# Performance work log

Measured on AMD Instinct MI355X. Metric: run time of the kernel, lower is better.

## Reference

```python
import jax, jax.numpy as jnp
import numpy as np
import math

N, E, R = 50000, 800000, 32
DIN = 128
H, D = 8, 16          # num_heads, head_dim; H*D == out_ent_feats == 128
HOP = 5
ALPHA = 0.1
EPS = 1e-5


def layer_norm(x, g, b):
    m = jnp.mean(x, axis=-1, keepdims=True)
    v = jnp.mean((x - m) ** 2, axis=-1, keepdims=True)
    return (x - m) * jax.lax.rsqrt(v + EPS) * g + b


def segment_softmax(e, dst, num_nodes):
    # e: [E, H] scores, softmax over incoming edges of each dst node
    m = jax.ops.segment_max(e, dst, num_segments=num_nodes)      # [N, H]
    ex = jnp.exp(e - m[dst])
    s = jax.ops.segment_sum(ex, dst, num_segments=num_nodes)     # [N, H]
    return ex / s[dst]


def setup_inputs() -> dict:
    key = jax.random.key(0)
    ks = jax.random.split(key, 12)
    gain = 0.02  # small init scale (small_init_gain-style)
    ent_feat = jax.random.normal(ks[0], (N, DIN), dtype=jnp.float32)
    rel_feat = jax.random.normal(ks[1], (R, DIN), dtype=jnp.float32)
    src = jax.random.randint(ks[2], (E,), 0, N, dtype=jnp.int32)
    # guarantee every node has in-degree >= 1 (DGL raises otherwise)
    dst_rand = jax.random.randint(ks[3], (E - N,), 0, N, dtype=jnp.int32)
    dst = jnp.concatenate([jnp.arange(N, dtype=jnp.int32), dst_rand])
    rid = jax.random.randint(ks[4], (E,), 0, R, dtype=jnp.int32)
    W_head = jax.random.normal(ks[5], (DIN, H * D), dtype=jnp.float32) * gain
    W_tail = jax.random.normal(ks[6], (DIN, H * D), dtype=jnp.float32) * gain
    W_ent = jax.random.normal(ks[7], (DIN, H * D), dtype=jnp.float32) * gain
    W_rel = jax.random.normal(ks[8], (DIN, H * D), dtype=jnp.float32) * gain
    attn_r = jax.random.normal(ks[9], (1, H, D), dtype=jnp.float32) * gain
    W1 = jax.random.normal(ks[10], (H * D, 4 * H * D), dtype=jnp.float32) * gain
    W2 = jax.random.normal(ks[11], (4 * H * D, H * D), dtype=jnp.float32) * gain
    return dict(
        ent_feat=ent_feat, rel_feat=rel_feat, src=src, dst=dst, rid=rid,
        W_head=W_head, W_tail=W_tail, W_ent=W_ent, W_rel=W_rel, attn_r=attn_r,
        ln_ent_g=jnp.ones((DIN,), jnp.float32), ln_ent_b=jnp.zeros((DIN,), jnp.float32),
        ln_rel_g=jnp.ones((DIN,), jnp.float32), ln_rel_b=jnp.zeros((DIN,), jnp.float32),
        ff_ln_g=jnp.ones((H * D,), jnp.float32), ff_ln_b=jnp.zeros((H * D,), jnp.float32),
        W1=W1, b1=jnp.zeros((4 * H * D,), jnp.float32),
        W2=W2, b2=jnp.zeros((H * D,), jnp.float32),
    )


def _forward(ent_feat, rel_feat, src, dst, rid,
             W_head, W_tail, W_ent, W_rel, attn_r,
             ln_ent_g, ln_ent_b, ln_rel_g, ln_rel_b, ff_ln_g, ff_ln_b,
             W1, b1, W2, b2):
    n = ent_feat.shape[0]
    x = layer_norm(ent_feat, ln_ent_g, ln_ent_b)
    feat_head = (x @ W_head).reshape(n, H, D)
    feat_tail = (x @ W_tail).reshape(n, H, D)
    feat_ent = (x @ W_ent).reshape(n, H, D)

    # per-edge dot-product attention score: u_dot_v('eh','et')
    e = jnp.sum(feat_head[src] * feat_tail[dst], axis=-1)          # [E, H]

    r = layer_norm(rel_feat, ln_rel_g, ln_rel_b)
    feat_rel = (r @ W_rel).reshape(R, H, D)
    er = jnp.sum(feat_rel * attn_r, axis=-1)                       # [R, H]
    e = e * er[rid]                                                # [E, H]

    # e_mul_v with log_in = log(in_degree) of dst node
    deg = jax.ops.segment_sum(jnp.ones((e.shape[0],), e.dtype), dst, num_segments=n)
    log_in = jnp.log(jnp.maximum(deg, 1.0))                        # [N]
    e = e * log_in[dst][:, None] / math.sqrt(D)

    a = segment_softmax(e, dst, n)                                 # [E, H]

    # PPR diffusion: feat <- (1-alpha) * A^T feat + alpha * feat_0
    feat = feat_ent
    for _ in range(HOP):
        msg = feat[src] * a[:, :, None]                            # [E, H, D]
        agg = jax.ops.segment_sum(msg, dst, num_segments=n)        # [N, H, D]
        feat = (1.0 - ALPHA) * agg + ALPHA * feat_ent

    # residual (Identity: in_ent_feats == out_ent_feats)
    rst = feat + ent_feat.reshape(n, H, D)
    rst = rst.reshape(n, H * D)

    h = layer_norm(rst, ff_ln_g, ff_ln_b)
    ff = jax.nn.relu(h @ W1 + b1) @ W2 + b2
    return ff + rst


def reference(ent_feat, rel_feat, src, dst, rid,
              W_head, W_tail, W_ent, W_rel, attn_r,
              ln_ent_g, ln_ent_b, ln_rel_g, ln_rel_b, ff_ln_g, ff_ln_b,
              W1, b1, W2, b2):
    return _forward(ent_feat, rel_feat, src, dst, rid,
                    W_head, W_tail, W_ent, W_rel, attn_r,
                    ln_ent_g, ln_ent_b, ln_rel_g, ln_rel_b, ff_ln_g, ff_ln_b,
                    W1, b1, W2, b2)
```

## Files before the change

### kernel.cpp

```cpp
#include <hip/hip_runtime.h>
#include <hip/hip_bf16.h>

#define N_NODES 50000
#define N_EDGES 800000
#define N_REL 32
#define DIN 128
#define NH 8
#define HD 16
#define FF_HID 512
#define EPS_LN 1e-5f
#define NBUCK 8
#define BDIV 6250
#define BCAP 114688

typedef __attribute__((ext_vector_type(8))) short bf16x8;
typedef __attribute__((ext_vector_type(4))) float f32x4;
typedef __attribute__((ext_vector_type(2))) float f32x2;
typedef unsigned short ushort_t;
typedef unsigned int uint_t;

static __device__ __forceinline__ unsigned short f2bf(float f) {
    union { float f; unsigned u; } v; v.f = f;
    unsigned r = (v.u + 0x7fffu + ((v.u >> 16) & 1u)) >> 16;
    return (unsigned short)r;
}
static __device__ __forceinline__ float bf2f(unsigned u16) {
    union { unsigned u; float f; } v; v.u = u16 << 16; return v.f;
}
static __device__ __forceinline__ unsigned char f2fp8(float f) {
    return (unsigned char)(__builtin_amdgcn_cvt_pk_fp8_f32(f, f, 0, false) & 0xff);
}
static __device__ __forceinline__ uint_t f2fp8x2(float x0, float x1) {
    return (__builtin_amdgcn_cvt_pk_fp8_f32(x0, x1, 0, false) & 0xffffu);
}

static __device__ __forceinline__ void pack_dev(const float* __restrict__ W,
                                                short* __restrict__ out, int K, int Ncols,
                                                int idx) {
    int KT = K >> 5;
    int l = idx & 63;
    int tile = idx >> 6;
    int kt = tile & (KT - 1);
    int ct = tile / KT;
    int c = ct * 16 + (l & 15);
    int k0 = kt * 32 + ((l >> 4) * 8);
    bf16x8 v;
#pragma unroll
    for (int j = 0; j < 8; j++) v[j] = (short)f2bf(W[(size_t)(k0 + j) * Ncols + c]);
    *(bf16x8*)(out + (size_t)idx * 8) = v;
}

#define C0_BIN 512
__global__ __launch_bounds__(256) void combo0_kernel(
    const int* __restrict__ src, const int* __restrict__ dst, const int* __restrict__ rid,
    int* __restrict__ deg, int* __restrict__ gcnt, int2* __restrict__ buck,
    const float* __restrict__ W1, short* __restrict__ W1p, const float* __restrict__ W2,
    short* __restrict__ W2p, const float* __restrict__ Wh, short* __restrict__ Whp,
    const float* __restrict__ Wt, short* __restrict__ Wtp, const float* __restrict__ We,
    short* __restrict__ Wep, const float* __restrict__ rel_feat,
    const float* __restrict__ gr, const float* __restrict__ br,
    const float* __restrict__ W_rel, const float* __restrict__ attn_r,
    float* __restrict__ er) {
    __shared__ float red[128];
    __shared__ float xsr[128];
    __shared__ float prod[128];
    __shared__ int cnt[NBUCK];
    __shared__ int sbase[NBUCK];
    int b = blockIdx.x, tid = threadIdx.x;
    if (b < C0_BIN) {
        const int chunk = (N_EDGES + C0_BIN - 1) / C0_BIN;
        int i0 = b * chunk;
        int i1 = min(i0 + chunk, N_EDGES);
        int rounds = (i1 - i0 + 255) >> 8;
        for (int r = 0; r < rounds; r++) {
            int i = i0 + (r << 8) + tid;
            if (tid < NBUCK) cnt[tid] = 0;
            __syncthreads();
            int d = 0, b8 = 0, rank = 0, py = 0;
            bool v = i < i1;
            if (v) {
                d = dst[i];
                b8 = d / BDIV;
                py = src[i] | (rid[i] << 16);
                rank = atomicAdd(&cnt[b8], 1);
                atomicAdd(&deg[d], 1);
            }
            __syncthreads();
            if (tid < NBUCK) sbase[tid] = atomicAdd(&gcnt[tid], cnt[tid]);
            __syncthreads();
            if (v) buck[(size_t)b8 * BCAP + sbase[b8] + rank] = make_int2(d, py);
            __syncthreads();
        }
    } else if (b < C0_BIN + 32) {
        pack_dev(W1, W1p, DIN, FF_HID, (b - C0_BIN) * 256 + tid);
    } else if (b < C0_BIN + 64) {
        pack_dev(W2, W2p, FF_HID, DIN, (b - C0_BIN - 32) * 256 + tid);
    } else if (b < C0_BIN + 72) {
        pack_dev(Wh, Whp, DIN, DIN, (b - C0_BIN - 64) * 256 + tid);
    } else if (b < C0_BIN + 80) {
        pack_dev(Wt, Wtp, DIN, DIN, (b - C0_BIN - 72) * 256 + tid);
    } else if (b < C0_BIN + 88) {
        pack_dev(We, Wep, DIN, DIN, (b - C0_BIN - 80) * 256 + tid);
    } else {
        int r = b - (C0_BIN + 88);
        float x = 0.f;
        if (tid < 128) {
            x = rel_feat[r * DIN + tid];
            red[tid] = x;
        }
        __syncthreads();
        for (int off = 64; off > 0; off >>= 1) {
            if (tid < off) red[tid] += red[tid + off];
            __syncthreads();
        }
        float mean = red[0] * (1.f / DIN);
        __syncthreads();
        if (tid < 128) red[tid] = x * x;
        __syncthreads();
        for (int off = 64; off > 0; off >>= 1) {
            if (tid < off) red[tid] += red[tid + off];
            __syncthreads();
        }
        float var = red[0] * (1.f / DIN) - mean * mean;
        float rs = rsqrtf(var + EPS_LN);
        if (tid < 128) xsr[tid] = (x - mean) * rs * gr[tid] + br[tid];
        __syncthreads();
        if (tid < 128) {
            float acc = 0.f;
            for (int k = 0; k < DIN; k++) acc += xsr[k] * W_rel[k * DIN + tid];
            prod[tid] = acc * attn_r[tid];
        }
        __syncthreads();
        if (tid < NH) {
            float s = 0.f;
            for (int d = 0; d < HD; d++) s += prod[tid * HD + d];
            er[r * NH + tid] = s;
        }
    }
}

__global__ __launch_bounds__(1024) void scan2_kernel(const int* __restrict__ deg,
                                                     int* __restrict__ row_off, int n) {
    __shared__ int lds[1024];
    __shared__ int wsum[16];
    __shared__ int s_base;
    int b = blockIdx.x, tid = threadIdx.x;
    int start = b * 1024;
    int partial = 0;
    for (int i = tid; i < start; i += 1024) partial += deg[i];
    for (int m = 32; m > 0; m >>= 1) partial += __shfl_down(partial, m);
    int wid = tid >> 6, lane = tid & 63;
    if (lane == 0) wsum[wid] = partial;
    __syncthreads();
    if (tid == 0) {
        int s = 0;
#pragma unroll
        for (int w = 0; w < 16; w++) s += wsum[w];
        s_base = s;
    }
    int i = start + tid;
    int v = (i < n) ? deg[i] : 0;
    lds[tid] = v;
    __syncthreads();
    for (int off = 1; off < 1024; off <<= 1) {
        int t = (tid >= off) ? lds[tid - off] : 0;
        __syncthreads();
        lds[tid] += t;
        __syncthreads();
    }
    int base = s_base;
    if (i < n) row_off[i] = base + lds[tid] - v;
    if (i == n - 1) row_off[n] = base + lds[tid];
}

#define C1_SCAT 1024
__global__ __launch_bounds__(256) void combo1_kernel(
    const int2* __restrict__ buck, const int* __restrict__ gcnt,
    const int* __restrict__ row_off, int* __restrict__ cursor, int* __restrict__ sr_perm,
    const float* __restrict__ ent, const float* __restrict__ g, const float* __restrict__ b,
    const short* __restrict__ Whp, const short* __restrict__ Wtp,
    const short* __restrict__ Wep, unsigned char* __restrict__ head_fp8,
    ushort_t* __restrict__ tail_bf, ushort_t* __restrict__ entp_bf,
    unsigned char* __restrict__ entp_fp8) {
    __shared__ float xs[32][128];
    __shared__ short hsb[32][136];
    int blk = blockIdx.x, tid = threadIdx.x;
    if (blk < C1_SCAT) {
        int b8 = blk & 7, sub = blk >> 3;
        int cnt = gcnt[b8];
        int chunk = (cnt + 127) >> 7;
        int i0 = sub * chunk;
        int i1 = min(i0 + chunk, cnt);
        const int2* bp = buck + (size_t)b8 * BCAP;
        for (int i = i0 + tid; i < i1; i += 256) {
            int2 e = bp[i];
            int p = row_off[e.x] + atomicAdd(&cursor[e.x], 1);
            sr_perm[p] = e.y;
        }
        return;
    }
    int base = (blk - C1_SCAT) * 32;
    {
        int c = tid & 127, rb = tid >> 7;
#pragma unroll
        for (int j = 0; j < 16; j++) {
            int r = j * 2 + rb;
            int row = base + r;
            xs[r][c] = (row < N_NODES) ? ent[(size_t)row * DIN + c] : 0.f;
        }
    }
    __syncthreads();
    int wave = tid >> 6, lane = tid & 63;
    {
        float g0 = g[lane], g1 = g[lane + 64], bb0 = b[lane], bb1 = b[lane + 64];
        for (int r = wave * 8; r < wave * 8 + 8; r++) {
            float x0 = xs[r][lane], x1 = xs[r][lane + 64];
            float s1 = x0 + x1, s2 = x0 * x0 + x1 * x1;
            for (int m = 1; m < 64; m <<= 1) {
                s1 += __shfl_xor(s1, m);
                s2 += __shfl_xor(s2, m);
            }
            float mean = s1 * (1.f / DIN);
            float var = s2 * (1.f / DIN) - mean * mean;
            float rs = rsqrtf(var + EPS_LN);
            hsb[r][lane] = (short)f2bf((x0 - mean) * rs * g0 + bb0);
            hsb[r][lane + 64] = (short)f2bf((x1 - mean) * rs * g1 + bb1);
        }
    }
    __syncthreads();
    bf16x8 a[2][4];
#pragma unroll
    for (int rt = 0; rt < 2; rt++)
#pragma unroll
        for (int kt = 0; kt < 4; kt++)
            a[rt][kt] = *(const bf16x8*)&hsb[rt * 16 + (lane & 15)][kt * 32 + (lane >> 4) * 8];
#pragma unroll
    for (int m = 0; m < 3; m++) {
        const bf16x8* bp = (m == 0)   ? (const bf16x8*)Whp
                           : (m == 1) ? (const bf16x8*)Wtp
                                      : (const bf16x8*)Wep;
#pragma unroll
        for (int c2 = 0; c2 < 2; c2++) {
            int ct = wave * 2 + c2;
            f32x4 acc0 = {0.f, 0.f, 0.f, 0.f}, acc1 = {0.f, 0.f, 0.f, 0.f};
#pragma unroll
            for (int kt = 0; kt < 4; kt++) {
                bf16x8 bf = bp[(ct * 4 + kt) * 64 + lane];
                acc0 = __builtin_amdgcn_mfma_f32_16x16x32_bf16(a[0][kt], bf, acc0, 0, 0, 0);
                acc1 = __builtin_amdgcn_mfma_f32_16x16x32_bf16(a[1][kt], bf, acc1, 0, 0, 0);
            }
            int col = ct * 16 + (lane & 15);
            int r0 = (lane >> 4) * 4;
#pragma unroll
            for (int j = 0; j < 4; j++) {
                int row0 = base + r0 + j, row1 = base + 16 + r0 + j;
                if (m == 0) {
                    if (row0 < N_NODES) head_fp8[(size_t)row0 * DIN + col] = f2fp8(acc0[j]);
                    if (row1 < N_NODES) head_fp8[(size_t)row1 * DIN + col] = f2fp8(acc1[j]);
                } else if (m == 1) {
                    if (row0 < N_NODES) tail_bf[(size_t)row0 * DIN + col] = f2bf(acc0[j]);
                    if (row1 < N_NODES) tail_bf[(size_t)row1 * DIN + col] = f2bf(acc1[j]);
                } else {
                    if (row0 < N_NODES) {
                        entp_bf[(size_t)row0 * DIN + col] = f2bf(acc0[j]);
                        entp_fp8[(size_t)row0 * DIN + col] = f2fp8(acc0[j]);
                    }
                    if (row1 < N_NODES) {
                        entp_bf[(size_t)row1 * DIN + col] = f2bf(acc1[j]);
                        entp_fp8[(size_t)row1 * DIN + col] = f2fp8(acc1[j]);
                    }
                }
            }
        }
    }
}

__global__ __launch_bounds__(256) void scores_kernel(
    const unsigned char* __restrict__ head_fp8, const ushort_t* __restrict__ tail_bf,
    const float* __restrict__ er, const int* __restrict__ row_off,
    const int* __restrict__ sr_perm, ushort_t* __restrict__ a_bf,
    float* __restrict__ inv9) {
    int wid = threadIdx.x >> 6;
    int u = blockIdx.x * 4 + wid;
    int lane = threadIdx.x & 63;
    int h = lane & 7, esub = lane >> 3;
    int p0 = row_off[u], p1 = row_off[u + 1];
    int deg = p1 - p0;
    float scale = logf((float)(deg > 0 ? deg : 1)) * 0.25f;
    float t[16];
    {
        const uint_t* tp = (const uint_t*)(tail_bf + (size_t)u * DIN + h * HD);
#pragma unroll
        for (int i = 0; i < 8; i++) {
            uint_t w = tp[i];
            t[2 * i] = bf2f(w & 0xffffu);
            t[2 * i + 1] = bf2f(w >> 16);
        }
    }
    float ssum = 0.f;
    for (int p = p0 + esub; p < p1; p += 8) {
        int v = sr_perm[p];
        int s = v & 0xffff;
        int rr = v >> 16;
        const uint_t* hp = (const uint_t*)(head_fp8 + (size_t)s * DIN + h * HD);
        float dot = 0.f;
#pragma unroll
        for (int i = 0; i < 4; i++) {
            uint_t w = hp[i];
            f32x2 lo = __builtin_amdgcn_cvt_pk_f32_fp8(w, false);
            f32x2 hi = __builtin_amdgcn_cvt_pk_f32_fp8(w, true);
            dot += lo.x * t[4 * i] + lo.y * t[4 * i + 1] + hi.x * t[4 * i + 2] +
                   hi.y * t[4 * i + 3];
        }
        float e = dot * er[rr * NH + h] * scale;
        float sx = expf(e);
        a_bf[(size_t)p * NH + h] = f2bf(sx);
        ssum += sx;
    }
    ssum += __shfl_xor(ssum, 8);
    ssum += __shfl_xor(ssum, 16);
    ssum += __shfl_xor(ssum, 32);
    if (lane < 8) inv9[(size_t)u * NH + lane] = 0.9f / ssum;
}

template <bool OUT_BF>
__global__ __launch_bounds__(256) void diffuse4_kernel(
    const unsigned char* __restrict__ fin8, const ushort_t* __restrict__ entp_bf,
    const ushort_t* __restrict__ a_bf, const int* __restrict__ sr_perm,
    const int* __restrict__ row_off, const float* __restrict__ inv9,
    void* __restrict__ fout) {
    int wid = threadIdx.x >> 6;
    int u = blockIdx.x * 4 + wid;
    int lane = threadIdx.x & 63;
    int c = lane & 15;
    int g = lane >> 4;
    int hh = c >> 1;
    int p0 = row_off[u], p1 = row_off[u + 1];
    float acc[8];
#pragma unroll
    for (int j = 0; j < 8; j++) acc[j] = 0.f;
    for (int p = p0; p < p1; p += 4) {
        int pe = p + g;
        bool valid = pe < p1;
        int pc = valid ? pe : (p1 - 1);
        int s = sr_perm[pc] & 0xffff;
        float a = valid ? bf2f(a_bf[(size_t)pc * NH + hh]) : 0.f;
        uint2 w = *(const uint2*)(fin8 + (size_t)s * DIN + 8 * c);
        f32x2 l0 = __builtin_amdgcn_cvt_pk_f32_fp8(w.x, false);
        f32x2 h0 = __builtin_amdgcn_cvt_pk_f32_fp8(w.x, true);
        f32x2 l1 = __builtin_amdgcn_cvt_pk_f32_fp8(w.y, false);
        f32x2 h1 = __builtin_amdgcn_cvt_pk_f32_fp8(w.y, true);
        acc[0] += a * l0.x; acc[1] += a * l0.y; acc[2] += a * h0.x; acc[3] += a * h0.y;
        acc[4] += a * l1.x; acc[5] += a * l1.y; acc[6] += a * h1.x; acc[7] += a * h1.y;
    }
#pragma unroll
    for (int j = 0; j < 8; j++) {
        acc[j] += __shfl_xor(acc[j], 16);
        acc[j] += __shfl_xor(acc[j], 32);
    }
    if (g == 0) {
        float iv = inv9[(size_t)u * NH + hh];
        size_t o = (size_t)u * DIN + 8 * c;
        uint4 e4 = *(const uint4*)(entp_bf + o);
        float x0 = iv * acc[0] + 0.1f * bf2f(e4.x & 0xffffu);
        float x1 = iv * acc[1] + 0.1f * bf2f(e4.x >> 16);
        float x2 = iv * acc[2] + 0.1f * bf2f(e4.y & 0xffffu);
        float x3 = iv * acc[3] + 0.1f * bf2f(e4.y >> 16);
        float x4 = iv * acc[4] + 0.1f * bf2f(e4.z & 0xffffu);
        float x5 = iv * acc[5] + 0.1f * bf2f(e4.z >> 16);
        float x6 = iv * acc[6] + 0.1f * bf2f(e4.w & 0xffffu);
        float x7 = iv * acc[7] + 0.1f * bf2f(e4.w >> 16);
        if (OUT_BF) {
            uint4 ov;
            ov.x = (uint_t)f2bf(x0) | ((uint_t)f2bf(x1) << 16);
            ov.y = (uint_t)f2bf(x2) | ((uint_t)f2bf(x3) << 16);
            ov.z = (uint_t)f2bf(x4) | ((uint_t)f2bf(x5) << 16);
            ov.w = (uint_t)f2bf(x6) | ((uint_t)f2bf(x7) << 16);
            *(uint4*)((ushort_t*)fout + o) = ov;
        } else {
            uint2 ov;
            ov.x = f2fp8x2(x0, x1) | (f2fp8x2(x2, x3) << 16);
            ov.y = f2fp8x2(x4, x5) | (f2fp8x2(x6, x7) << 16);
            *(uint2*)((unsigned char*)fout + o) = ov;
        }
    }
}

static __device__ __forceinline__ int hid_idx(int row, int col) {
    return row * 512 + ((((col >> 3) & 63) ^ (row & 7)) << 3) + (col & 7);
}
__global__ __launch_bounds__(256) void ffn_mfma_kernel(
    const ushort_t* __restrict__ feat, const float* __restrict__ ent0,
    const float* __restrict__ g, const float* __restrict__ b,
    const short* __restrict__ W1p, const float* __restrict__ b1,
    const short* __restrict__ W2p, const float* __restrict__ b2,
    float* __restrict__ out) {
    __shared__ ushort_t rst_bf[16][136];
    __shared__ short hs[16][136];
    __shared__ short hid[16 * 512];
    int tid = threadIdx.x;
    int base = blockIdx.x * 16;
    int wave = tid >> 6, lane = tid & 63;
    {
        int c = tid & 127, rb = tid >> 7;
#pragma unroll
        for (int j = 0; j < 8; j++) {
            int r = j * 2 + rb;
            int row = base + r;
            float v = 0.f;
            if (row < N_NODES) {
                size_t idx = (size_t)row * DIN + c;
                v = bf2f(feat[idx]) + ent0[idx];
            }
            rst_bf[r][c] = f2bf(v);
        }
    }
    __syncthreads();
    {
        float g0 = g[lane], g1 = g[lane + 64], bb0 = b[lane], bb1 = b[lane + 64];
        for (int r = wave * 4; r < wave * 4 + 4; r++) {
            float x0 = bf2f(rst_bf[r][lane]), x1 = bf2f(rst_bf[r][lane + 64]);
            float s1 = x0 + x1, s2 = x0 * x0 + x1 * x1;
            for (int m = 1; m < 64; m <<= 1) {
                s1 += __shfl_xor(s1, m);
                s2 += __shfl_xor(s2, m);
            }
            float mean = s1 * (1.f / DIN);
            float var = s2 * (1.f / DIN) - mean * mean;
            float rs = rsqrtf(var + EPS_LN);
            hs[r][lane] = (short)f2bf((x0 - mean) * rs * g0 + bb0);
            hs[r][lane + 64] = (short)f2bf((x1 - mean) * rs * g1 + bb1);
        }
    }
    __syncthreads();
    {
        bf16x8 a[4];
#pragma unroll
        for (int kt = 0; kt < 4; kt++)
            a[kt] = *(const bf16x8*)&hs[lane & 15][kt * 32 + (lane >> 4) * 8];
        const bf16x8* bp = (const bf16x8*)W1p;
        for (int cti = 0; cti < 8; cti++) {
            int ct = wave * 8 + cti;
            f32x4 acc0 = {0.f, 0.f, 0.f, 0.f};
#pragma unroll
            for (int kt = 0; kt < 4; kt++) {
                bf16x8 bf = bp[(ct * 4 + kt) * 64 + lane];
                acc0 = __builtin_amdgcn_mfma_f32_16x16x32_bf16(a[kt], bf, acc0, 0, 0, 0);
            }
            int col = ct * 16 + (lane & 15);
            float bv = b1[col];
            int r0 = (lane >> 4) * 4;
#pragma unroll
            for (int j = 0; j < 4; j++)
                hid[hid_idx(r0 + j, col)] = (short)f2bf(fmaxf(acc0[j] + bv, 0.f));
        }
    }
    __syncthreads();
    {
        f32x4 acc[2] = {{0.f, 0.f, 0.f, 0.f}, {0.f, 0.f, 0.f, 0.f}};
        const bf16x8* bp2 = (const bf16x8*)W2p;
        for (int kt = 0; kt < 16; kt++) {
            int col8 = kt * 32 + (lane >> 4) * 8;
            bf16x8 a0 = *(const bf16x8*)&hid[hid_idx(lane & 15, col8)];
#pragma unroll
            for (int c2 = 0; c2 < 2; c2++) {
                int ct = wave * 2 + c2;
                bf16x8 bf = bp2[(ct * 16 + kt) * 64 + lane];
                acc[c2] = __builtin_amdgcn_mfma_f32_16x16x32_bf16(a0, bf, acc[c2], 0, 0, 0);
            }
        }
#pragma unroll
        for (int c2 = 0; c2 < 2; c2++) {
            int col = (wave * 2 + c2) * 16 + (lane & 15);
            float bv = b2[col];
            int r0 = (lane >> 4) * 4;
#pragma unroll
            for (int j = 0; j < 4; j++) {
                int row = base + r0 + j;
                if (row < N_NODES)
                    out[(size_t)row * DIN + col] = acc[c2][j] + bv + bf2f(rst_bf[r0 + j][col]);
            }
        }
    }
}

extern "C" void kernel_launch(void* const* d_in, const int* in_sizes, int n_in,
                              void* d_out, int out_size, void* d_ws, size_t ws_size,
                              hipStream_t stream) {
    const float* ent_feat = (const float*)d_in[0];
    const float* rel_feat = (const float*)d_in[1];
    const int* src = (const int*)d_in[2];
    const int* dst = (const int*)d_in[3];
    const int* rid = (const int*)d_in[4];
    const float* W_head = (const float*)d_in[5];
    const float* W_tail = (const float*)d_in[6];
    const float* W_ent = (const float*)d_in[7];
    const float* W_rel = (const float*)d_in[8];
    const float* attn_r = (const float*)d_in[9];
    const float* ln_ent_g = (const float*)d_in[10];
    const float* ln_ent_b = (const float*)d_in[11];
    const float* ln_rel_g = (const float*)d_in[12];
    const float* ln_rel_b = (const float*)d_in[13];
    const float* ff_ln_g = (const float*)d_in[14];
    const float* ff_ln_b = (const float*)d_in[15];
    const float* W1 = (const float*)d_in[16];
    const float* b1 = (const float*)d_in[17];
    const float* W2 = (const float*)d_in[18];
    const float* b2 = (const float*)d_in[19];
    float* out = (float*)d_out;

    const int N = N_NODES, E = N_EDGES;

    char* cur = (char*)d_ws;
    auto alloc = [&](size_t bytes, size_t align) -> void* {
        uintptr_t p = (uintptr_t)cur;
        p = (p + align - 1) & ~(uintptr_t)(align - 1);
        cur = (char*)(p + bytes);
        return (void*)p;
    };
    ushort_t* tail_bf = (ushort_t*)alloc((size_t)N * DIN * 2, 16);
    ushort_t* entp_bf = (ushort_t*)alloc((size_t)N * DIN * 2, 16);
    unsigned char* entp_fp8 = (unsigned char*)alloc((size_t)N * DIN, 16);
    unsigned char* f8A = (unsigned char*)alloc((size_t)N * DIN, 16);
    unsigned char* f8B = (unsigned char*)alloc((size_t)N * DIN, 16);
    unsigned char* head_fp8 = (unsigned char*)alloc((size_t)N * DIN, 16);
    int2* buck = (int2*)alloc((size_t)NBUCK * BCAP * 8, 16);
    int* sr_perm = (int*)alloc((size_t)E * 4, 16);
    int* row_off = (int*)alloc((size_t)(N + 1) * 4, 16);
    int* deg = (int*)alloc(((size_t)2 * N + NBUCK) * 4, 16);
    int* cursor = deg + N;
    int* gcnt = deg + 2 * N;
    float* er = (float*)alloc((size_t)N_REL * NH * 4, 16);
    float* inv9 = (float*)alloc((size_t)N * NH * 4, 16);
    short* W1p = (short*)alloc((size_t)DIN * FF_HID * 2, 16);
    short* W2p = (short*)alloc((size_t)FF_HID * DIN * 2, 16);
    short* Whp = (short*)alloc((size_t)DIN * DIN * 2, 16);
    short* Wtp = (short*)alloc((size_t)DIN * DIN * 2, 16);
    short* Wep = (short*)alloc((size_t)DIN * DIN * 2, 16);
    ushort_t* a_fit = (ushort_t*)alloc((size_t)E * NH * 2, 16);
    ushort_t* a_bf = ((size_t)(cur - (char*)d_ws) <= ws_size) ? a_fit : (ushort_t*)d_out;

    hipMemsetAsync(deg, 0, sizeof(int) * ((size_t)2 * N + NBUCK), stream);
    combo0_kernel<<<632, 256, 0, stream>>>(src, dst, rid, deg, gcnt, buck, W1, W1p, W2,
                                           W2p, W_head, Whp, W_tail, Wtp, W_ent, Wep,
                                           rel_feat, ln_rel_g, ln_rel_b, W_rel, attn_r,
                                           er);
    scan2_kernel<<<(N + 1023) / 1024, 1024, 0, stream>>>(deg, row_off, N);
    int nblk32 = (N + 31) / 32;
    combo1_kernel<<<C1_SCAT + nblk32, 256, 0, stream>>>(
        buck, gcnt, row_off, cursor, sr_perm, ent_feat, ln_ent_g, ln_ent_b, Whp, Wtp,
        Wep, head_fp8, tail_bf, entp_bf, entp_fp8);
    scores_kernel<<<N / 4, 256, 0, stream>>>(head_fp8, tail_bf, er, row_off, sr_perm,
                                             a_bf, inv9);
    diffuse4_kernel<false><<<N / 4, 256, 0, stream>>>(entp_fp8, entp_bf, a_bf, sr_perm,
                                                      row_off, inv9, f8A);
    diffuse4_kernel<false><<<N / 4, 256, 0, stream>>>(f8A, entp_bf, a_bf, sr_perm,
                                                      row_off, inv9, f8B);
    diffuse4_kernel<false><<<N / 4, 256, 0, stream>>>(f8B, entp_bf, a_bf, sr_perm,
                                                      row_off, inv9, f8A);
    diffuse4_kernel<false><<<N / 4, 256, 0, stream>>>(f8A, entp_bf, a_bf, sr_perm,
                                                      row_off, inv9, f8B);
    diffuse4_kernel<true><<<N / 4, 256, 0, stream>>>(f8B, entp_bf, a_bf, sr_perm,
                                                     row_off, inv9, tail_bf);
    int nblk16 = (N + 15) / 16;
    ffn_mfma_kernel<<<nblk16, 256, 0, stream>>>(tail_bf, ent_feat, ff_ln_g, ff_ln_b, W1p,
                                                b1, W2p, b2, out);
}
```

Baseline: 369.2 us.

## Fuse first diffusion hop into score kernel and interleave head/ent fp8 layout

```diff
diff --git a/kernel.cpp b/kernel.cpp
--- a/kernel.cpp
+++ b/kernel.cpp
@@ -32,6 +32,11 @@
 }
 static __device__ __forceinline__ uint_t f2fp8x2(float x0, float x1) {
     return (__builtin_amdgcn_cvt_pk_fp8_f32(x0, x1, 0, false) & 0xffffu);
+}
+static __device__ __forceinline__ void fp8x4_to_f32(uint_t w, float* o) {
+    f32x2 lo = __builtin_amdgcn_cvt_pk_f32_fp8(w, false);
+    f32x2 hi = __builtin_amdgcn_cvt_pk_f32_fp8(w, true);
+    o[0] = lo.x; o[1] = lo.y; o[2] = hi.x; o[3] = hi.y;
 }
 
 static __device__ __forceinline__ void pack_dev(const float* __restrict__ W,
@@ -139,67 +144,43 @@
     }
 }
 
-__global__ __launch_bounds__(1024) void scan2_kernel(const int* __restrict__ deg,
-                                                     int* __restrict__ row_off, int n) {
-    __shared__ int lds[1024];
-    __shared__ int wsum[16];
-    __shared__ int s_base;
-    int b = blockIdx.x, tid = threadIdx.x;
-    int start = b * 1024;
-    int partial = 0;
-    for (int i = tid; i < start; i += 1024) partial += deg[i];
-    for (int m = 32; m > 0; m >>= 1) partial += __shfl_down(partial, m);
-    int wid = tid >> 6, lane = tid & 63;
-    if (lane == 0) wsum[wid] = partial;
-    __syncthreads();
-    if (tid == 0) {
-        int s = 0;
-#pragma unroll
-        for (int w = 0; w < 16; w++) s += wsum[w];
-        s_base = s;
-    }
-    int i = start + tid;
-    int v = (i < n) ? deg[i] : 0;
-    lds[tid] = v;
-    __syncthreads();
-    for (int off = 1; off < 1024; off <<= 1) {
-        int t = (tid >= off) ? lds[tid - off] : 0;
-        __syncthreads();
-        lds[tid] += t;
-        __syncthreads();
-    }
-    int base = s_base;
-    if (i < n) row_off[i] = base + lds[tid] - v;
-    if (i == n - 1) row_off[n] = base + lds[tid];
-}
-
-#define C1_SCAT 1024
-__global__ __launch_bounds__(256) void combo1_kernel(
-    const int2* __restrict__ buck, const int* __restrict__ gcnt,
-    const int* __restrict__ row_off, int* __restrict__ cursor, int* __restrict__ sr_perm,
+#define NS_SCAN 196
+__global__ __launch_bounds__(256) void combo_mid_kernel(
+    const int* __restrict__ deg, int* __restrict__ row_off,
     const float* __restrict__ ent, const float* __restrict__ g, const float* __restrict__ b,
     const short* __restrict__ Whp, const short* __restrict__ Wtp,
-    const short* __restrict__ Wep, unsigned char* __restrict__ head_fp8,
-    ushort_t* __restrict__ tail_bf, ushort_t* __restrict__ entp_bf,
-    unsigned char* __restrict__ entp_fp8) {
+    const short* __restrict__ Wep, unsigned char* __restrict__ hent,
+    ushort_t* __restrict__ tail_bf) {
     __shared__ float xs[32][128];
     __shared__ short hsb[32][136];
     int blk = blockIdx.x, tid = threadIdx.x;
-    if (blk < C1_SCAT) {
-        int b8 = blk & 7, sub = blk >> 3;
-        int cnt = gcnt[b8];
-        int chunk = (cnt + 127) >> 7;
-        int i0 = sub * chunk;
-        int i1 = min(i0 + chunk, cnt);
-        const int2* bp = buck + (size_t)b8 * BCAP;
-        for (int i = i0 + tid; i < i1; i += 256) {
-            int2 e = bp[i];
-            int p = row_off[e.x] + atomicAdd(&cursor[e.x], 1);
-            sr_perm[p] = e.y;
-        }
+    if (blk < NS_SCAN) {
+        __shared__ int lscan[256];
+        __shared__ int ws4[4];
+        int n = N_NODES;
+        int start = blk * 256;
+        int partial = 0;
+        for (int i = tid; i < start; i += 256) partial += deg[i];
+        for (int m = 32; m > 0; m >>= 1) partial += __shfl_down(partial, m);
+        int wid = tid >> 6, lane = tid & 63;
+        if (lane == 0) ws4[wid] = partial;
+        __syncthreads();
+        int sbase = ws4[0] + ws4[1] + ws4[2] + ws4[3];
+        int i = start + tid;
+        int v = (i < n) ? deg[i] : 0;
+        lscan[tid] = v;
+        __syncthreads();
+        for (int off = 1; off < 256; off <<= 1) {
+            int t = (tid >= off) ? lscan[tid - off] : 0;
+            __syncthreads();
+            lscan[tid] += t;
+            __syncthreads();
+        }
+        if (i < n) row_off[i] = sbase + lscan[tid] - v;
+        if (i == n - 1) row_off[n] = sbase + lscan[tid];
         return;
     }
-    int base = (blk - C1_SCAT) * 32;
+    int base = (blk - NS_SCAN) * 32;
     {
         int c = tid & 127, rb = tid >> 7;
 #pragma unroll
@@ -250,36 +231,50 @@
                 acc1 = __builtin_amdgcn_mfma_f32_16x16x32_bf16(a[1][kt], bf, acc1, 0, 0, 0);
             }
             int col = ct * 16 + (lane & 15);
+            int h = col >> 4, k = col & 15;
             int r0 = (lane >> 4) * 4;
 #pragma unroll
             for (int j = 0; j < 4; j++) {
                 int row0 = base + r0 + j, row1 = base + 16 + r0 + j;
                 if (m == 0) {
-                    if (row0 < N_NODES) head_fp8[(size_t)row0 * DIN + col] = f2fp8(acc0[j]);
-                    if (row1 < N_NODES) head_fp8[(size_t)row1 * DIN + col] = f2fp8(acc1[j]);
+                    if (row0 < N_NODES) hent[(size_t)row0 * 256 + h * 32 + k] = f2fp8(acc0[j]);
+                    if (row1 < N_NODES) hent[(size_t)row1 * 256 + h * 32 + k] = f2fp8(acc1[j]);
                 } else if (m == 1) {
                     if (row0 < N_NODES) tail_bf[(size_t)row0 * DIN + col] = f2bf(acc0[j]);
                     if (row1 < N_NODES) tail_bf[(size_t)row1 * DIN + col] = f2bf(acc1[j]);
                 } else {
-                    if (row0 < N_NODES) {
-                        entp_bf[(size_t)row0 * DIN + col] = f2bf(acc0[j]);
-                        entp_fp8[(size_t)row0 * DIN + col] = f2fp8(acc0[j]);
-                    }
-                    if (row1 < N_NODES) {
-                        entp_bf[(size_t)row1 * DIN + col] = f2bf(acc1[j]);
-                        entp_fp8[(size_t)row1 * DIN + col] = f2fp8(acc1[j]);
-                    }
+                    if (row0 < N_NODES)
+                        hent[(size_t)row0 * 256 + h * 32 + 16 + k] = f2fp8(acc0[j]);
+                    if (row1 < N_NODES)
+                        hent[(size_t)row1 * 256 + h * 32 + 16 + k] = f2fp8(acc1[j]);
                 }
             }
         }
     }
 }
 
-__global__ __launch_bounds__(256) void scores_kernel(
-    const unsigned char* __restrict__ head_fp8, const ushort_t* __restrict__ tail_bf,
+__global__ __launch_bounds__(256) void scatter_kernel(
+    const int2* __restrict__ buck, const int* __restrict__ gcnt,
+    const int* __restrict__ row_off, int* __restrict__ cursor, int* __restrict__ sr_perm) {
+    int blk = blockIdx.x, tid = threadIdx.x;
+    int b8 = blk & 7, sub = blk >> 3;
+    int cnt = gcnt[b8];
+    int chunk = (cnt + 127) >> 7;
+    int i0 = sub * chunk;
+    int i1 = min(i0 + chunk, cnt);
+    const int2* bp = buck + (size_t)b8 * BCAP;
+    for (int i = i0 + tid; i < i1; i += 256) {
+        int2 e = bp[i];
+        int p = row_off[e.x] + atomicAdd(&cursor[e.x], 1);
+        sr_perm[p] = e.y;
+    }
+}
+
+__global__ __launch_bounds__(256) void score_hop_kernel(
+    const unsigned char* __restrict__ hent, const ushort_t* __restrict__ tail_bf,
     const float* __restrict__ er, const int* __restrict__ row_off,
     const int* __restrict__ sr_perm, ushort_t* __restrict__ a_bf,
-    float* __restrict__ inv9) {
+    float* __restrict__ inv9, unsigned char* __restrict__ fout) {
     int wid = threadIdx.x >> 6;
     int u = blockIdx.x * 4 + wid;
     int lane = threadIdx.x & 63;
@@ -298,34 +293,62 @@
         }
     }
     float ssum = 0.f;
+    float acc[16];
+#pragma unroll
+    for (int k = 0; k < 16; k++) acc[k] = 0.f;
     for (int p = p0 + esub; p < p1; p += 8) {
         int v = sr_perm[p];
         int s = v & 0xffff;
         int rr = v >> 16;
-        const uint_t* hp = (const uint_t*)(head_fp8 + (size_t)s * DIN + h * HD);
+        const uint4* hp = (const uint4*)(hent + (size_t)s * 256 + h * 32);
+        uint4 hw = hp[0];
+        uint4 ew = hp[1];
+        float hv[16], ev[16];
+        fp8x4_to_f32(hw.x, hv + 0); fp8x4_to_f32(hw.y, hv + 4);
+        fp8x4_to_f32(hw.z, hv + 8); fp8x4_to_f32(hw.w, hv + 12);
+        fp8x4_to_f32(ew.x, ev + 0); fp8x4_to_f32(ew.y, ev + 4);
+        fp8x4_to_f32(ew.z, ev + 8); fp8x4_to_f32(ew.w, ev + 12);
         float dot = 0.f;
 #pragma unroll
-        for (int i = 0; i < 4; i++) {
-            uint_t w = hp[i];
-            f32x2 lo = __builtin_amdgcn_cvt_pk_f32_fp8(w, false);
-            f32x2 hi = __builtin_amdgcn_cvt_pk_f32_fp8(w, true);
-            dot += lo.x * t[4 * i] + lo.y * t[4 * i + 1] + hi.x * t[4 * i + 2] +
-                   hi.y * t[4 * i + 3];
-        }
+        for (int k = 0; k < 16; k++) dot += t[k] * hv[k];
         float e = dot * er[rr * NH + h] * scale;
         float sx = expf(e);
         a_bf[(size_t)p * NH + h] = f2bf(sx);
         ssum += sx;
+#pragma unroll
+        for (int k = 0; k < 16; k++) acc[k] += sx * ev[k];
     }
     ssum += __shfl_xor(ssum, 8);
     ssum += __shfl_xor(ssum, 16);
     ssum += __shfl_xor(ssum, 32);
-    if (lane < 8) inv9[(size_t)u * NH + lane] = 0.9f / ssum;
+#pragma unroll
+    for (int k = 0; k < 16; k++) {
+        acc[k] += __shfl_xor(acc[k], 8);
+        acc[k] += __shfl_xor(acc[k], 16);
+        acc[k] += __shfl_xor(acc[k], 32);
+    }
+    if (esub == 0) {
+        float iv = 0.9f / ssum;
+        inv9[(size_t)u * NH + h] = iv;
+        const uint4 eu = *(const uint4*)(hent + (size_t)u * 256 + h * 32 + 16);
+        float e0[16];
+        fp8x4_to_f32(eu.x, e0 + 0); fp8x4_to_f32(eu.y, e0 + 4);
+        fp8x4_to_f32(eu.z, e0 + 8); fp8x4_to_f32(eu.w, e0 + 12);
+        float x[16];
+#pragma unroll
+        for (int k = 0; k < 16; k++) x[k] = iv * acc[k] + 0.1f * e0[k];
+        uint4 ov;
+        ov.x = f2fp8x2(x[0], x[1]) | (f2fp8x2(x[2], x[3]) << 16);
+        ov.y = f2fp8x2(x[4], x[5]) | (f2fp8x2(x[6], x[7]) << 16);
+        ov.z = f2fp8x2(x[8], x[9]) | (f2fp8x2(x[10], x[11]) << 16);
+        ov.w = f2fp8x2(x[12], x[13]) | (f2fp8x2(x[14], x[15]) << 16);
+        *(uint4*)(fout + (size_t)u * DIN + h * HD) = ov;
+    }
 }
 
 template <bool OUT_BF>
 __global__ __launch_bounds__(256) void diffuse4_kernel(
-    const unsigned char* __restrict__ fin8, const ushort_t* __restrict__ entp_bf,
+    const unsigned char* __restrict__ fin8, const unsigned char* __restrict__ hent,
     const ushort_t* __restrict__ a_bf, const int* __restrict__ sr_perm,
     const int* __restrict__ row_off, const float* __restrict__ inv9,
     void* __restrict__ fout) {
@@ -346,12 +369,11 @@
         int s = sr_perm[pc] & 0xffff;
         float a = valid ? bf2f(a_bf[(size_t)pc * NH + hh]) : 0.f;
         uint2 w = *(const uint2*)(fin8 + (size_t)s * DIN + 8 * c);
-        f32x2 l0 = __builtin_amdgcn_cvt_pk_f32_fp8(w.x, false);
-        f32x2 h0 = __builtin_amdgcn_cvt_pk_f32_fp8(w.x, true);
-        f32x2 l1 = __builtin_amdgcn_cvt_pk_f32_fp8(w.y, false);
-        f32x2 h1 = __builtin_amdgcn_cvt_pk_f32_fp8(w.y, true);
-        acc[0] += a * l0.x; acc[1] += a * l0.y; acc[2] += a * h0.x; acc[3] += a * h0.y;
-        acc[4] += a * l1.x; acc[5] += a * l1.y; acc[6] += a * h1.x; acc[7] += a * h1.y;
+        float v[8];
+        fp8x4_to_f32(w.x, v + 0);
+        fp8x4_to_f32(w.y, v + 4);
+#pragma unroll
+        for (int j = 0; j < 8; j++) acc[j] += a * v[j];
     }
 #pragma unroll
     for (int j = 0; j < 8; j++) {
@@ -360,27 +382,25 @@
     }
     if (g == 0) {
         float iv = inv9[(size_t)u * NH + hh];
+        uint2 ew = *(const uint2*)(hent + (size_t)u * 256 + hh * 32 + 16 + (c & 1) * 8);
+        float e0[8];
+        fp8x4_to_f32(ew.x, e0 + 0);
+        fp8x4_to_f32(ew.y, e0 + 4);
+        float x[8];
+#pragma unroll
+        for (int j = 0; j < 8; j++) x[j] = iv * acc[j] + 0.1f * e0[j];
         size_t o = (size_t)u * DIN + 8 * c;
-        uint4 e4 = *(const uint4*)(entp_bf + o);
-        float x0 = iv * acc[0] + 0.1f * bf2f(e4.x & 0xffffu);
-        float x1 = iv * acc[1] + 0.1f * bf2f(e4.x >> 16);
-        float x2 = iv * acc[2] + 0.1f * bf2f(e4.y & 0xffffu);
-        float x3 = iv * acc[3] + 0.1f * bf2f(e4.y >> 16);
-        float x4 = iv * acc[4] + 0.1f * bf2f(e4.z & 0xffffu);
-        float x5 = iv * acc[5] + 0.1f * bf2f(e4.z >> 16);
-        float x6 = iv * acc[6] + 0.1f * bf2f(e4.w & 0xffffu);
-        float x7 = iv * acc[7] + 0.1f * bf2f(e4.w >> 16);
         if (OUT_BF) {
             uint4 ov;
-            ov.x = (uint_t)f2bf(x0) | ((uint_t)f2bf(x1) << 16);
-            ov.y = (uint_t)f2bf(x2) | ((uint_t)f2bf(x3) << 16);
-            ov.z = (uint_t)f2bf(x4) | ((uint_t)f2bf(x5) << 16);
-            ov.w = (uint_t)f2bf(x6) | ((uint_t)f2bf(x7) << 16);
+            ov.x = (uint_t)f2bf(x[0]) | ((uint_t)f2bf(x[1]) << 16);
+            ov.y = (uint_t)f2bf(x[2]) | ((uint_t)f2bf(x[3]) << 16);
+            ov.z = (uint_t)f2bf(x[4]) | ((uint_t)f2bf(x[5]) << 16);
+            ov.w = (uint_t)f2bf(x[6]) | ((uint_t)f2bf(x[7]) << 16);
             *(uint4*)((ushort_t*)fout + o) = ov;
         } else {
             uint2 ov;
-            ov.x = f2fp8x2(x0, x1) | (f2fp8x2(x2, x3) << 16);
-            ov.y = f2fp8x2(x4, x5) | (f2fp8x2(x6, x7) << 16);
+            ov.x = f2fp8x2(x[0], x[1]) | (f2fp8x2(x[2], x[3]) << 16);
+            ov.y = f2fp8x2(x[4], x[5]) | (f2fp8x2(x[6], x[7]) << 16);
             *(uint2*)((unsigned char*)fout + o) = ov;
         }
     }
@@ -519,11 +539,9 @@
         return (void*)p;
     };
     ushort_t* tail_bf = (ushort_t*)alloc((size_t)N * DIN * 2, 16);
-    ushort_t* entp_bf = (ushort_t*)alloc((size_t)N * DIN * 2, 16);
-    unsigned char* entp_fp8 = (unsigned char*)alloc((size_t)N * DIN, 16);
+    unsigned char* hent = (unsigned char*)alloc((size_t)N * 256, 16);
     unsigned char* f8A = (unsigned char*)alloc((size_t)N * DIN, 16);
     unsigned char* f8B = (unsigned char*)alloc((size_t)N * DIN, 16);
-    unsigned char* head_fp8 = (unsigned char*)alloc((size_t)N * DIN, 16);
     int2* buck = (int2*)alloc((size_t)NBUCK * BCAP * 8, 16);
     int* sr_perm = (int*)alloc((size_t)E * 4, 16);
     int* row_off = (int*)alloc((size_t)(N + 1) * 4, 16);
@@ -545,23 +563,20 @@
                                            W2p, W_head, Whp, W_tail, Wtp, W_ent, Wep,
                                            rel_feat, ln_rel_g, ln_rel_b, W_rel, attn_r,
                                            er);
-    scan2_kernel<<<(N + 1023) / 1024, 1024, 0, stream>>>(deg, row_off, N);
     int nblk32 = (N + 31) / 32;
-    combo1_kernel<<<C1_SCAT + nblk32, 256, 0, stream>>>(
-        buck, gcnt, row_off, cursor, sr_perm, ent_feat, ln_ent_g, ln_ent_b, Whp, Wtp,
-        Wep, head_fp8, tail_bf, entp_bf, entp_fp8);
-    scores_kernel<<<N / 4, 256, 0, stream>>>(head_fp8, tail_bf, er, row_off, sr_perm,
-                                             a_bf, inv9);
-    diffuse4_kernel<false><<<N / 4, 256, 0, stream>>>(entp_fp8, entp_bf, a_bf, sr_perm,
-                                                      row_off, inv9, f8A);
-    diffuse4_kernel<false><<<N / 4, 256, 0, stream>>>(f8A, entp_bf, a_bf, sr_perm,
-                                                      row_off, inv9, f8B);
-    diffuse4_kernel<false><<<N / 4, 256, 0, stream>>>(f8B, entp_bf, a_bf, sr_perm,
-                                                      row_off, inv9, f8A);
-    diffuse4_kernel<false><<<N / 4, 256, 0, stream>>>(f8A, entp_bf, a_bf, sr_perm,
-                                                      row_off, inv9, f8B);
-    diffuse4_kernel<true><<<N / 4, 256, 0, stream>>>(f8B, entp_bf, a_bf, sr_perm,
-                                                     row_off, inv9, tail_bf);
+    combo_mid_kernel<<<NS_SCAN + nblk32, 256, 0, stream>>>(
+        deg, row_off, ent_feat, ln_ent_g, ln_ent_b, Whp, Wtp, Wep, hent, tail_bf);
+    scatter_kernel<<<1024, 256, 0, stream>>>(buck, gcnt, row_off, cursor, sr_perm);
+    score_hop_kernel<<<N / 4, 256, 0, stream>>>(hent, tail_bf, er, row_off, sr_perm,
+                                                a_bf, inv9, f8A);
+    diffuse4_kernel<false><<<N / 4, 256, 0, stream>>>(f8A, hent, a_bf, sr_perm, row_off,
+                                                      inv9, f8B);
+    diffuse4_kernel<false><<<N / 4, 256, 0, stream>>>(f8B, hent, a_bf, sr_perm, row_off,
+                                                      inv9, f8A);
+    diffuse4_kernel<false><<<N / 4, 256, 0, stream>>>(f8A, hent, a_bf, sr_perm, row_off,
+                                                      inv9, f8B);
+    diffuse4_kernel<true><<<N / 4, 256, 0, stream>>>(f8B, hent, a_bf, sr_perm, row_off,
+                                                     inv9, tail_bf);
     int nblk16 = (N + 15) / 16;
     ffn_mfma_kernel<<<nblk16, 256, 0, stream>>>(tail_bf, ent_feat, ff_ln_g, ff_ln_b, W1p,
                                                 b1, W2p, b2, out);
```

Measured after the change: 355.8 us. 3.6% less time.
